# Kernel optimization log

Hardware: AMD Instinct MI355X
Metric: run time of the kernel (lower is better)

Reference implementation:

```python
import jax, jax.numpy as jnp
import numpy as np

EMBED = 512
WINDOW = 64

def setup_inputs() -> dict:
    key = jax.random.key(0)
    ks = jax.random.split(key, 5)
    B, S, E = 4, 4096, EMBED
    s = 1.0 / np.sqrt(E)
    x = jax.random.normal(ks[0], (B, S, E), dtype=jnp.float32)
    W_qkv = jax.random.uniform(ks[1], (E, 3 * E), minval=-s, maxval=s, dtype=jnp.float32)
    b_qkv = jax.random.uniform(ks[2], (3 * E,), minval=-s, maxval=s, dtype=jnp.float32)
    W_out = jax.random.uniform(ks[3], (E, E), minval=-s, maxval=s, dtype=jnp.float32)
    b_out = jax.random.uniform(ks[4], (E,), minval=-s, maxval=s, dtype=jnp.float32)
    return {"x": x, "W_qkv": W_qkv, "b_qkv": b_qkv, "W_out": W_out, "b_out": b_out}

def reference(x, W_qkv, b_qkv, W_out, b_out):
    B, S, E = x.shape
    scale = jnp.sqrt(jnp.asarray(E, dtype=x.dtype))
    qkv = x @ W_qkv + b_qkv                    # [B,S,3E]
    q, k, v = jnp.split(qkv, 3, axis=-1)       # each [B,S,E]
    scores = jnp.einsum('bqe,bke->bqk', q, k) / scale  # [B,S,S]
    pos = jnp.arange(S)
    dist = pos[None, :] - pos[:, None]         # [S,S]
    window_mask = jnp.abs(dist) <= WINDOW
    neg_inf = jnp.asarray(-jnp.inf, dtype=scores.dtype)
    scores = jnp.where(window_mask[None, :, :], scores, neg_inf)
    attn = jax.nn.softmax(scores, axis=-1)     # every row has in-window entries
    attended = jnp.einsum('bqk,bke->bqe', attn, v)
    return attended @ W_out + b_out
```

## Files before the change

### kernel.cpp

```cpp
#include <hip/hip_runtime.h>

typedef __attribute__((ext_vector_type(8))) _Float16 f16x8;
typedef __attribute__((ext_vector_type(4))) _Float16 f16x4;
typedef __attribute__((ext_vector_type(4))) float f32x4;
typedef __attribute__((address_space(1))) const char gc_char;
typedef __attribute__((address_space(3))) char ls_char;

#define MFMA(a, b, c) __builtin_amdgcn_mfma_f32_16x16x32_f16((a), (b), (c), 0, 0, 0)
#define FENCE() asm volatile("" ::: "memory")
#define BARRIER() do { FENCE(); __builtin_amdgcn_s_barrier(); FENCE(); } while (0)
#define VMW(n) asm volatile("s_waitcnt vmcnt(" #n ")" ::: "memory")

static constexpr int SEQ = 4096;
static constexpr int EMB = 512;
static constexpr float QSCALE = 0.04419417382415922f;

__device__ __forceinline__ void gl_lds16(const void* g, void* l) {
    __builtin_amdgcn_global_load_lds((gc_char*)g, (ls_char*)l, 16, 0, 0);
}

__global__ void k_prep(const float* __restrict__ x, _Float16* __restrict__ xb,
                       const float* __restrict__ Wq, _Float16* __restrict__ WqT,
                       const float* __restrict__ Wo, _Float16* __restrict__ WoT) {
    const int bid = blockIdx.x, tid = threadIdx.x;
    if (bid < 4096) {
        long i = (long)bid * 256 + tid;
        const float4* p = (const float4*)x + i * 2;
        float4 a = p[0], b = p[1];
        f16x8 v;
        v[0] = (_Float16)a.x; v[1] = (_Float16)a.y; v[2] = (_Float16)a.z; v[3] = (_Float16)a.w;
        v[4] = (_Float16)b.x; v[5] = (_Float16)b.y; v[6] = (_Float16)b.z; v[7] = (_Float16)b.w;
        *(f16x8*)(xb + i * 8) = v;
    } else {
        __shared__ float Ls[64][65];
        int t = bid - 4096;
        const float* W; _Float16* WT; int N, k0, n0;
        if (t < 192) { W = Wq; WT = WqT; N = 1536; k0 = (t & 7) * 64; n0 = (t >> 3) * 64; }
        else { t -= 192; W = Wo; WT = WoT; N = 512; k0 = (t & 7) * 64; n0 = (t >> 3) * 64; }
        int c = tid & 63, r4 = tid >> 6;
#pragma unroll
        for (int i = 0; i < 16; ++i) {
            int row = i * 4 + r4;
            Ls[row][c] = W[(long)(k0 + row) * N + n0 + c];
        }
        __syncthreads();
#pragma unroll
        for (int i = 0; i < 16; ++i) {
            int row = i * 4 + r4;
            WT[(long)(n0 + row) * 512 + k0 + c] = (_Float16)Ls[c][row];
        }
    }
}

__launch_bounds__(512, 2) __global__
void k_gemm_qkv(const _Float16* __restrict__ A, const _Float16* __restrict__ BT,
                const float* __restrict__ bias,
                _Float16* __restrict__ Qo, _Float16* __restrict__ Ko, _Float16* __restrict__ VT) {
    extern __shared__ __align__(16) char smem[];
    const int tid = threadIdx.x, w = tid >> 6, lane = tid & 63, g = lane >> 4, f = lane & 15;
    const int wrow = w >> 2, wcol = w & 3;
    const int bid = blockIdx.x;
    const int swz = (bid & 7) * 48 + (bid >> 3);
    const int brow = swz / 6, bcol = swz - brow * 6;
    const long row0 = (long)brow * 256;
    const int col0 = bcol * 256;
    const char* Abase = (const char*)A + row0 * 1024;
    const char* Bbase = (const char*)BT + (long)col0 * 1024;

    f32x4 acc[8][4] = {};
    f16x8 a[4][2], b[2][2];

    auto stageA = [&](int h, char* dstbuf, int kt) {
#pragma unroll
        for (int it = 0; it < 2; ++it) {
            int s = it * 512 + tid;
            int lr = s >> 3;
            int ch = (s & 7) ^ (lr & 7);
            int r = (lr & 63) | ((lr & 64) << 1) | (h << 6);
            gl_lds16(Abase + (long)r * 1024 + kt * 128 + ch * 16, dstbuf + h * 16384 + s * 16);
        }
    };
    auto stageB = [&](int h, char* dstbuf, int kt) {
#pragma unroll
        for (int it = 0; it < 2; ++it) {
            int s = it * 512 + tid;
            int lr = s >> 3;
            int ch = (s & 7) ^ (lr & 7);
            int n = (lr & 31) | ((lr >> 5) << 6) | (h << 5);
            gl_lds16(Bbase + (long)n * 1024 + kt * 128 + ch * 16, dstbuf + h * 16384 + s * 16);
        }
    };
    auto ldA = [&](const char* buf, int mq) {
#pragma unroll
        for (int mi = 0; mi < 4; ++mi)
#pragma unroll
            for (int ks = 0; ks < 2; ++ks) {
                int r = wrow * 128 + mq * 64 + mi * 16 + f;
                int half = (r >> 6) & 1, lr = (r & 63) | ((r & 128) >> 1);
                int cl = ks * 4 + g;
                a[mi][ks] = *(const f16x8*)(buf + half * 16384 + lr * 128 + ((cl ^ (lr & 7)) << 4));
            }
    };
    auto ldB = [&](const char* buf, int nq) {
#pragma unroll
        for (int ni = 0; ni < 2; ++ni)
#pragma unroll
            for (int ks = 0; ks < 2; ++ks) {
                int n = wcol * 64 + nq * 32 + ni * 16 + f;
                int half = (n >> 5) & 1, lr = (n & 31) | (((n >> 6) & 3) << 5);
                int cl = ks * 4 + g;
                b[ni][ks] = *(const f16x8*)(buf + half * 16384 + lr * 128 + ((cl ^ (lr & 7)) << 4));
            }
    };
    auto mfma16 = [&](int mq, int nq) {
        __builtin_amdgcn_s_setprio(1);
#pragma unroll
        for (int mi = 0; mi < 4; ++mi)
#pragma unroll
            for (int ni = 0; ni < 2; ++ni)
#pragma unroll
                for (int ks = 0; ks < 2; ++ks)
                    acc[mq * 4 + mi][nq * 2 + ni] = MFMA(a[mi][ks], b[ni][ks], acc[mq * 4 + mi][nq * 2 + ni]);
        __builtin_amdgcn_s_setprio(0);
    };

    {
        char* A0 = smem;
        char* B0 = smem + 32768;
        stageA(0, A0, 0); stageB(0, B0, 0); stageB(1, B0, 0); stageA(1, A0, 0);
    }
    VMW(4);
    BARRIER();

    for (int kt = 0; kt < 8; ++kt) {
        const char* Ac = smem + (kt & 1) * 65536;
        const char* Bc = Ac + 32768;
        char* An = smem + ((kt + 1) & 1) * 65536;
        char* Bn = An + 32768;
        const bool last = (kt == 7);
        ldA(Ac, 0); ldB(Bc, 0);
        if (!last) stageA(0, An, kt + 1);
        BARRIER();
        mfma16(0, 0);
        if (!last) { VMW(4); } else { VMW(2); }
        BARRIER();
        ldB(Bc, 1);
        if (!last) stageB(0, Bn, kt + 1);
        BARRIER();
        mfma16(0, 1);
        if (!last) { VMW(4); } else { VMW(0); }
        BARRIER();
        ldA(Ac, 1); ldB(Bc, 0);
        if (!last) stageB(1, Bn, kt + 1);
        BARRIER();
        mfma16(1, 0);
        BARRIER();
        ldB(Bc, 1);
        if (!last) stageA(1, An, kt + 1);
        BARRIER();
        mfma16(1, 1);
        if (!last) { VMW(4); }
        BARRIER();
    }

    float bv[4];
#pragma unroll
    for (int ni = 0; ni < 4; ++ni) bv[ni] = bias[col0 + wcol * 64 + ni * 16 + f];

    if (col0 >= 1024) {
#pragma unroll
        for (int mi = 0; mi < 8; ++mi)
#pragma unroll
            for (int ni = 0; ni < 4; ++ni) {
                int r0 = wrow * 128 + mi * 16 + g * 4;
                int c = wcol * 64 + ni * 16 + f;
                f16x4 v4;
#pragma unroll
                for (int j = 0; j < 4; ++j) v4[j] = (_Float16)(acc[mi][ni][j] + bv[ni]);
                *(f16x4*)(smem + c * 512 + ((r0 * 2) ^ ((c & 7) << 4))) = v4;
            }
        __syncthreads();
        int bb = (int)(row0 >> 12);
        _Float16* vt = VT + ((long)bb * 512 + (col0 - 1024)) * 4096 + (row0 & 4095);
#pragma unroll
        for (int it = 0; it < 16; ++it) {
            int e = it * 16 + (tid >> 5);
            int ch = tid & 31;
            f16x8 v = *(const f16x8*)(smem + e * 512 + ((ch * 16) ^ ((e & 7) << 4)));
            *(f16x8*)(vt + (long)e * 4096 + ch * 8) = v;
        }
    } else {
        const float sc = (col0 < 512) ? QSCALE : 1.0f;
#pragma unroll
        for (int mi = 0; mi < 8; ++mi)
#pragma unroll
            for (int ni = 0; ni < 4; ++ni)
#pragma unroll
                for (int j = 0; j < 4; ++j) {
                    int r = wrow * 128 + mi * 16 + g * 4 + j;
                    int c = wcol * 64 + ni * 16 + f;
                    float v = (acc[mi][ni][j] + bv[ni]) * sc;
                    int pc = ((c >> 3) + ((r >> 2) & 7) * 2) & 31;
                    *(_Float16*)(smem + r * 512 + pc * 16 + (c & 7) * 2) = (_Float16)v;
                }
        __syncthreads();
        _Float16* dst = (col0 < 512) ? Qo : Ko;
        int cofs = (col0 < 512) ? col0 : col0 - 512;
#pragma unroll
        for (int it = 0; it < 16; ++it) {
            int r = it * 16 + (tid >> 5);
            int ch = tid & 31;
            int pc = (ch + ((r >> 2) & 7) * 2) & 31;
            f16x8 v = *(const f16x8*)(smem + r * 512 + pc * 16);
            *(f16x8*)(dst + (row0 + r) * 512 + cofs + ch * 8) = v;
        }
    }
}

__launch_bounds__(256, 2) __global__
void k_gemm_out(const _Float16* __restrict__ A, const _Float16* __restrict__ BT,
                const float* __restrict__ bias, float* __restrict__ out) {
    __shared__ __align__(16) _Float16 As[128 * 64];
    __shared__ __align__(16) _Float16 Bs[128 * 64];
    const int tid = threadIdx.x, w = tid >> 6, lane = tid & 63, g = lane >> 4, f = lane & 15;
    const int wr = w >> 1, wc = w & 1;
    const long row0 = (long)blockIdx.x * 128, col0 = (long)blockIdx.y * 128;
    f32x4 acc[4][4] = {};
    const char* Ab = (const char*)(A + row0 * 512);
    const char* Bb = (const char*)(BT + col0 * 512);

    for (int kt = 0; kt < 8; ++kt) {
        __syncthreads();
        const char* Asrc = Ab + kt * 128;
        const char* Bsrc = Bb + kt * 128;
#pragma unroll
        for (int it = 0; it < 4; ++it) {
            int slot = it * 256 + tid;
            int r = slot >> 3, ch = slot & 7;
            int scol = (ch * 16) ^ ((r & 7) << 4);
            gl_lds16(Asrc + (long)r * 1024 + scol, (char*)As + (it * 256 + (tid & 0xC0)) * 16);
            gl_lds16(Bsrc + (long)r * 1024 + scol, (char*)Bs + (it * 256 + (tid & 0xC0)) * 16);
        }
        __syncthreads();
#pragma unroll
        for (int ks = 0; ks < 2; ++ks) {
            f16x8 af[4], bf[4];
#pragma unroll
            for (int mi = 0; mi < 4; ++mi) {
                int r = wr * 64 + mi * 16 + f;
                af[mi] = *(const f16x8*)((const char*)As + r * 128 + ((ks * 64 + g * 16) ^ ((r & 7) << 4)));
            }
#pragma unroll
            for (int ni = 0; ni < 4; ++ni) {
                int r = wc * 64 + ni * 16 + f;
                bf[ni] = *(const f16x8*)((const char*)Bs + r * 128 + ((ks * 64 + g * 16) ^ ((r & 7) << 4)));
            }
#pragma unroll
            for (int mi = 0; mi < 4; ++mi)
#pragma unroll
                for (int ni = 0; ni < 4; ++ni)
                    acc[mi][ni] = MFMA(af[mi], bf[ni], acc[mi][ni]);
        }
    }
#pragma unroll
    for (int mi = 0; mi < 4; ++mi)
#pragma unroll
        for (int ni = 0; ni < 4; ++ni) {
            long r0 = row0 + wr * 64 + mi * 16 + g * 4;
            int c = (int)col0 + wc * 64 + ni * 16 + f;
            float bv = bias[c];
#pragma unroll
            for (int j = 0; j < 4; ++j)
                out[(r0 + j) * 512 + c] = acc[mi][ni][j] + bv;
        }
}

__launch_bounds__(512, 1) __global__
void k_attn(const _Float16* __restrict__ Qb, const _Float16* __restrict__ Kb,
            const _Float16* __restrict__ VT, _Float16* __restrict__ Ob) {
    extern __shared__ __align__(16) char smem[];
    char* buf[2] = { smem, smem + 49152 };
    char* Pl = smem + 98304;
    float* Mp = (float*)(smem + 123904);
    float* Lp = (float*)(smem + 124928);

    const int tid = threadIdx.x, w = tid >> 6, lane = tid & 63, g = lane >> 4, f = lane & 15;
    const int rh = w >> 2, kh = w & 3;
    const int bid = blockIdx.x;
    const int swzb = (bid & 7) * 32 + (bid >> 3);
    const int b = swzb >> 6, qt = swzb & 63;
    const int q0 = qt * 64, kbase = q0 - 64;
    const long bofs = (long)b * SEQ;

    f16x8 qf[2][16];
#pragma unroll
    for (int mt = 0; mt < 2; ++mt) {
        const _Float16* qr = Qb + (bofs + q0 + rh * 32 + mt * 16 + f) * EMB + g * 8;
#pragma unroll
        for (int ks = 0; ks < 16; ++ks) qf[mt][ks] = *(const f16x8*)(qr + ks * 32);
    }

    auto stageK = [&](int ec, char* dst) {
#pragma unroll
        for (int it = 0; it < 6; ++it) {
            int slot = it * 512 + tid;
            int r = slot >> 4, c = slot & 15;
            int cs = c ^ (r & 7);
            int key = min(max(kbase + r, 0), SEQ - 1);
            gl_lds16(Kb + (bofs + key) * EMB + ec * 128 + cs * 8, dst + slot * 16);
        }
    };
    auto stageVT = [&](int ec, char* dst) {
#pragma unroll
        for (int it = 0; it < 6; ++it) {
            int slot = it * 512 + tid;
            int r = slot / 24, c = slot - r * 24;
            int cs = c ^ (r & 7);
            int k0 = min(max(kbase + cs * 8, 0), SEQ - 8);
            gl_lds16(VT + ((long)b * 512 + ec * 128 + r) * 4096 + k0, dst + slot * 16);
        }
    };

    f32x4 sacc[2][3] = {};
    stageK(0, buf[0]);
    __syncthreads();
    for (int ec = 0; ec < 4; ++ec) {
        if (ec < 3) stageK(ec + 1, buf[(ec + 1) & 1]);
        else stageVT(0, buf[0]);
        const char* kb = buf[ec & 1];
#pragma unroll
        for (int kk = 0; kk < 4; ++kk) {
#pragma unroll
            for (int t = 0; t < 3; ++t) {
                int n = kh * 48 + t * 16 + f;
                f16x8 bf = *(const f16x8*)(kb + n * 256 + (((kk * 4 + g) ^ (n & 7)) << 4));
#pragma unroll
                for (int mt = 0; mt < 2; ++mt)
                    sacc[mt][t] = MFMA(qf[mt][ec * 4 + kk], bf, sacc[mt][t]);
            }
        }
        __syncthreads();
    }

    float m[2][4] = {{-3e30f, -3e30f, -3e30f, -3e30f}, {-3e30f, -3e30f, -3e30f, -3e30f}};
    float l[2][4] = {};
#pragma unroll
    for (int mt = 0; mt < 2; ++mt)
#pragma unroll
        for (int t = 0; t < 3; ++t) {
            int key = kbase + kh * 48 + t * 16 + f;
            bool kv = (key >= 0) && (key < SEQ);
#pragma unroll
            for (int j = 0; j < 4; ++j) {
                int d = key - (q0 + rh * 32 + mt * 16 + g * 4 + j);
                bool valid = kv && (d >= -64) && (d <= 64);
                float s = valid ? sacc[mt][t][j] : -3e30f;
                sacc[mt][t][j] = s;
                m[mt][j] = fmaxf(m[mt][j], s);
            }
        }
#pragma unroll
    for (int mt = 0; mt < 2; ++mt)
#pragma unroll
        for (int j = 0; j < 4; ++j) {
            m[mt][j] = fmaxf(m[mt][j], __shfl_xor(m[mt][j], 1));
            m[mt][j] = fmaxf(m[mt][j], __shfl_xor(m[mt][j], 2));
            m[mt][j] = fmaxf(m[mt][j], __shfl_xor(m[mt][j], 4));
            m[mt][j] = fmaxf(m[mt][j], __shfl_xor(m[mt][j], 8));
        }
    if (f == 0) {
#pragma unroll
        for (int mt = 0; mt < 2; ++mt)
#pragma unroll
            for (int j = 0; j < 4; ++j)
                Mp[kh * 64 + rh * 32 + mt * 16 + g * 4 + j] = m[mt][j];
    }
    __syncthreads();
#pragma unroll
    for (int mt = 0; mt < 2; ++mt)
#pragma unroll
        for (int j = 0; j < 4; ++j) {
            int r = rh * 32 + mt * 16 + g * 4 + j;
            m[mt][j] = fmaxf(fmaxf(Mp[r], Mp[64 + r]), fmaxf(Mp[128 + r], Mp[192 + r]));
        }
#pragma unroll
    for (int mt = 0; mt < 2; ++mt)
#pragma unroll
        for (int t = 0; t < 3; ++t)
#pragma unroll
            for (int j = 0; j < 4; ++j) {
                float p = __expf(sacc[mt][t][j] - m[mt][j]);
                sacc[mt][t][j] = p;
                l[mt][j] += p;
            }
#pragma unroll
    for (int mt = 0; mt < 2; ++mt)
#pragma unroll
        for (int j = 0; j < 4; ++j) {
            l[mt][j] += __shfl_xor(l[mt][j], 1);
            l[mt][j] += __shfl_xor(l[mt][j], 2);
            l[mt][j] += __shfl_xor(l[mt][j], 4);
            l[mt][j] += __shfl_xor(l[mt][j], 8);
        }
    if (f == 0) {
#pragma unroll
        for (int mt = 0; mt < 2; ++mt)
#pragma unroll
            for (int j = 0; j < 4; ++j)
                Lp[kh * 64 + rh * 32 + mt * 16 + g * 4 + j] = l[mt][j];
    }
#pragma unroll
    for (int mt = 0; mt < 2; ++mt)
#pragma unroll
        for (int t = 0; t < 3; ++t)
#pragma unroll
            for (int j = 0; j < 4; ++j)
                *(_Float16*)(Pl + (rh * 32 + mt * 16 + g * 4 + j) * 400 +
                             (kh * 48 + t * 16 + f) * 2) = (_Float16)sacc[mt][t][j];
    __syncthreads();

    float rl[2][4];
#pragma unroll
    for (int mt = 0; mt < 2; ++mt)
#pragma unroll
        for (int j = 0; j < 4; ++j) {
            int r = rh * 32 + mt * 16 + g * 4 + j;
            rl[mt][j] = 1.0f / (Lp[r] + Lp[64 + r] + Lp[128 + r] + Lp[192 + r]);
        }

    f16x8 pf[2][6];
#pragma unroll
    for (int mt = 0; mt < 2; ++mt)
#pragma unroll
        for (int kc = 0; kc < 6; ++kc)
            pf[mt][kc] = *(const f16x8*)(Pl + (rh * 32 + mt * 16 + f) * 400 + kc * 64 + g * 16);

    for (int ec = 0; ec < 4; ++ec) {
        if (ec < 3) stageVT(ec + 1, buf[(ec + 1) & 1]);
        const char* vb = buf[ec & 1];
        f32x4 o[2][2] = {};
#pragma unroll
        for (int kc = 0; kc < 6; ++kc) {
#pragma unroll
            for (int nt = 0; nt < 2; ++nt) {
                int e = kh * 32 + nt * 16 + f;
                f16x8 vf = *(const f16x8*)(vb + e * 384 + (((kc * 4 + g) ^ (e & 7)) << 4));
#pragma unroll
                for (int mt = 0; mt < 2; ++mt)
                    o[mt][nt] = MFMA(pf[mt][kc], vf, o[mt][nt]);
            }
        }
#pragma unroll
        for (int mt = 0; mt < 2; ++mt)
#pragma unroll
            for (int nt = 0; nt < 2; ++nt) {
                _Float16* ob = Ob + (bofs + q0 + rh * 32 + mt * 16 + g * 4) * EMB +
                               ec * 128 + kh * 32 + nt * 16 + f;
#pragma unroll
                for (int j = 0; j < 4; ++j)
                    ob[(long)j * EMB] = (_Float16)(o[mt][nt][j] * rl[mt][j]);
            }
        if (ec < 3) __syncthreads();
    }
}

extern "C" void kernel_launch(void* const* d_in, const int* in_sizes, int n_in,
                              void* d_out, int out_size, void* d_ws, size_t ws_size,
                              hipStream_t stream) {
    const float* x     = (const float*)d_in[0];
    const float* W_qkv = (const float*)d_in[1];
    const float* b_qkv = (const float*)d_in[2];
    const float* W_out = (const float*)d_in[3];
    const float* b_out = (const float*)d_in[4];

    char* ws = (char*)d_ws;
    _Float16* xb    = (_Float16*)(ws);
    _Float16* WqkvT = (_Float16*)(ws + 16777216);
    _Float16* WoutT = (_Float16*)(ws + 16777216 + 1572864);
    _Float16* Qb    = (_Float16*)(ws + 18874368);
    _Float16* Kb    = (_Float16*)(ws + 18874368 + 16777216);
    _Float16* VT    = (_Float16*)(ws + 18874368 + 33554432);
    _Float16* Ob    = xb;
    float* out = (float*)d_out;

    (void)hipFuncSetAttribute((const void*)k_gemm_qkv,
                              hipFuncAttributeMaxDynamicSharedMemorySize, 131072);
    (void)hipFuncSetAttribute((const void*)k_attn,
                              hipFuncAttributeMaxDynamicSharedMemorySize, 126976);

    k_prep<<<4352, 256, 0, stream>>>(x, xb, W_qkv, WqkvT, W_out, WoutT);
    k_gemm_qkv<<<384, 512, 131072, stream>>>(xb, WqkvT, b_qkv, Qb, Kb, VT);
    k_attn<<<256, 512, 125952, stream>>>(Qb, Kb, VT, Ob);
    dim3 g2(128, 4);
    k_gemm_out<<<g2, 256, 0, stream>>>(Ob, WoutT, b_out, out);
}
```

Measured before the change: 87.61 us.

## Unify GEMMs into templated 128x256-tile pipelined kernel for QKV and output projections

Replaces the QKV GEMM (256x256 tiles, 384 blocks) and the simple output GEMM with one templated kernel that uses 128x256 tiles and a double-buffered global_load_lds pipeline. The QKV projection now launches 768 blocks to fill more CUs, and the output projection gains the async staged pipeline in place of its synchronous per-k-step loads. In exchange each tile reuses its operands less and issues more loads per FLOP, and occupancy is set to one block per CU.

```diff
diff --git a/kernel.cpp b/kernel.cpp
--- a/kernel.cpp
+++ b/kernel.cpp
@@ -52,227 +52,175 @@
     }
 }
 
-__launch_bounds__(512, 2) __global__
-void k_gemm_qkv(const _Float16* __restrict__ A, const _Float16* __restrict__ BT,
-                const float* __restrict__ bias,
-                _Float16* __restrict__ Qo, _Float16* __restrict__ Ko, _Float16* __restrict__ VT) {
+template <int NCT, int EPI>
+__launch_bounds__(512, 1) __global__
+void k_gemm2(const _Float16* __restrict__ A, const _Float16* __restrict__ BT,
+             const float* __restrict__ bias, void* o0, void* o1, void* o2) {
     extern __shared__ __align__(16) char smem[];
-    const int tid = threadIdx.x, w = tid >> 6, lane = tid & 63, g = lane >> 4, f = lane & 15;
+    const int tid = threadIdx.x, lane = tid & 63, w = tid >> 6, g = lane >> 4, f = lane & 15;
     const int wrow = w >> 2, wcol = w & 3;
     const int bid = blockIdx.x;
-    const int swz = (bid & 7) * 48 + (bid >> 3);
-    const int brow = swz / 6, bcol = swz - brow * 6;
-    const long row0 = (long)brow * 256;
+    constexpr int NBLK = 128 * NCT;
+    const int swz = (bid & 7) * (NBLK / 8) + (bid >> 3);
+    const int brow = swz / NCT, bcol = swz - brow * NCT;
+    const long row0 = (long)brow * 128;
     const int col0 = bcol * 256;
     const char* Abase = (const char*)A + row0 * 1024;
     const char* Bbase = (const char*)BT + (long)col0 * 1024;
 
-    f32x4 acc[8][4] = {};
-    f16x8 a[4][2], b[2][2];
-
-    auto stageA = [&](int h, char* dstbuf, int kt) {
+    f32x4 acc[4][4] = {};
+    f16x8 a[2][2], breg[2][2][2];
+
+    auto stageA = [&](int h, char* dst, int kt) {
+        int rr = tid >> 3;
+        int ch = (tid & 7) ^ (rr & 7);
+        int grow = h * 32 + (rr & 31) + (rr >> 5) * 64;
+        gl_lds16(Abase + (long)grow * 1024 + kt * 128 + ch * 16, dst + h * 8192 + tid * 16);
+    };
+    auto stageB = [&](int h, char* dst, int kt) {
 #pragma unroll
         for (int it = 0; it < 2; ++it) {
             int s = it * 512 + tid;
-            int lr = s >> 3;
-            int ch = (s & 7) ^ (lr & 7);
-            int r = (lr & 63) | ((lr & 64) << 1) | (h << 6);
-            gl_lds16(Abase + (long)r * 1024 + kt * 128 + ch * 16, dstbuf + h * 16384 + s * 16);
-        }
-    };
-    auto stageB = [&](int h, char* dstbuf, int kt) {
-#pragma unroll
-        for (int it = 0; it < 2; ++it) {
-            int s = it * 512 + tid;
-            int lr = s >> 3;
-            int ch = (s & 7) ^ (lr & 7);
-            int n = (lr & 31) | ((lr >> 5) << 6) | (h << 5);
-            gl_lds16(Bbase + (long)n * 1024 + kt * 128 + ch * 16, dstbuf + h * 16384 + s * 16);
-        }
-    };
-    auto ldA = [&](const char* buf, int mq) {
+            int cc = s >> 3;
+            int ch = (s & 7) ^ (cc & 7);
+            int gcol = h * 32 + (cc & 31) + (cc >> 5) * 64;
+            gl_lds16(Bbase + (long)gcol * 1024 + kt * 128 + ch * 16,
+                     dst + 16384 + h * 16384 + s * 16);
+        }
+    };
+    auto ldA = [&](const char* buf, int mh) {
+#pragma unroll
+        for (int mi = 0; mi < 2; ++mi)
+#pragma unroll
+            for (int ks = 0; ks < 2; ++ks) {
+                int rr = wrow * 32 + mi * 16 + f;
+                int cl = ks * 4 + g;
+                a[mi][ks] = *(const f16x8*)(buf + mh * 8192 + rr * 128 + ((cl ^ (rr & 7)) << 4));
+            }
+    };
+    auto ldB = [&](const char* buf, int nh) {
+#pragma unroll
+        for (int ni = 0; ni < 2; ++ni)
+#pragma unroll
+            for (int ks = 0; ks < 2; ++ks) {
+                int cc = wcol * 32 + ni * 16 + f;
+                int cl = ks * 4 + g;
+                breg[nh][ni][ks] =
+                    *(const f16x8*)(buf + 16384 + nh * 16384 + cc * 128 + ((cl ^ (cc & 7)) << 4));
+            }
+    };
+    auto mfma8 = [&](int mh, int nh) {
+        __builtin_amdgcn_s_setprio(1);
+#pragma unroll
+        for (int mi = 0; mi < 2; ++mi)
+#pragma unroll
+            for (int ni = 0; ni < 2; ++ni)
+#pragma unroll
+                for (int ks = 0; ks < 2; ++ks)
+                    acc[mh * 2 + mi][nh * 2 + ni] =
+                        MFMA(a[mi][ks], breg[nh][ni][ks], acc[mh * 2 + mi][nh * 2 + ni]);
+        __builtin_amdgcn_s_setprio(0);
+    };
+
+    stageB(0, smem, 0);
+    stageA(0, smem, 0); stageA(1, smem, 0);
+    stageB(1, smem, 0);
+    VMW(3);
+    BARRIER();
+
+    for (int kt = 0; kt < 8; ++kt) {
+        const char* cur = smem + (kt & 1) * 49152;
+        char* nxt = smem + ((kt + 1) & 1) * 49152;
+        const bool last = (kt == 7);
+        ldA(cur, 0); ldB(cur, 0);
+        if (!last) stageB(0, nxt, kt + 1);
+        BARRIER();
+        mfma8(0, 0);
+        if (!last) { VMW(2); } else { VMW(0); }
+        BARRIER();
+        ldB(cur, 1);
+        if (!last) { stageA(0, nxt, kt + 1); stageA(1, nxt, kt + 1); }
+        BARRIER();
+        mfma8(0, 1);
+        BARRIER();
+        ldA(cur, 1);
+        if (!last) stageB(1, nxt, kt + 1);
+        BARRIER();
+        mfma8(1, 0);
+        BARRIER();
+        mfma8(1, 1);
+        if (!last) { VMW(3); }
+        BARRIER();
+    }
+
+    if (EPI == 1) {
+        float* out = (float*)o0;
 #pragma unroll
         for (int mi = 0; mi < 4; ++mi)
 #pragma unroll
-            for (int ks = 0; ks < 2; ++ks) {
-                int r = wrow * 128 + mq * 64 + mi * 16 + f;
-                int half = (r >> 6) & 1, lr = (r & 63) | ((r & 128) >> 1);
-                int cl = ks * 4 + g;
-                a[mi][ks] = *(const f16x8*)(buf + half * 16384 + lr * 128 + ((cl ^ (lr & 7)) << 4));
-            }
-    };
-    auto ldB = [&](const char* buf, int nq) {
-#pragma unroll
-        for (int ni = 0; ni < 2; ++ni)
-#pragma unroll
-            for (int ks = 0; ks < 2; ++ks) {
-                int n = wcol * 64 + nq * 32 + ni * 16 + f;
-                int half = (n >> 5) & 1, lr = (n & 31) | (((n >> 6) & 3) << 5);
-                int cl = ks * 4 + g;
-                b[ni][ks] = *(const f16x8*)(buf + half * 16384 + lr * 128 + ((cl ^ (lr & 7)) << 4));
-            }
-    };
-    auto mfma16 = [&](int mq, int nq) {
-        __builtin_amdgcn_s_setprio(1);
+            for (int ni = 0; ni < 4; ++ni) {
+                long r0 = row0 + wrow * 64 + mi * 16 + g * 4;
+                int c = col0 + wcol * 64 + ni * 16 + f;
+                float bv = bias[c];
+#pragma unroll
+                for (int j = 0; j < 4; ++j)
+                    out[(r0 + j) * 512 + c] = acc[mi][ni][j] + bv;
+            }
+        return;
+    }
+
+    float bv[4];
+#pragma unroll
+    for (int ni = 0; ni < 4; ++ni) bv[ni] = bias[col0 + wcol * 64 + ni * 16 + f];
+
+    if (col0 >= 1024) {
 #pragma unroll
         for (int mi = 0; mi < 4; ++mi)
 #pragma unroll
-            for (int ni = 0; ni < 2; ++ni)
-#pragma unroll
-                for (int ks = 0; ks < 2; ++ks)
-                    acc[mq * 4 + mi][nq * 2 + ni] = MFMA(a[mi][ks], b[ni][ks], acc[mq * 4 + mi][nq * 2 + ni]);
-        __builtin_amdgcn_s_setprio(0);
-    };
-
-    {
-        char* A0 = smem;
-        char* B0 = smem + 32768;
-        stageA(0, A0, 0); stageB(0, B0, 0); stageB(1, B0, 0); stageA(1, A0, 0);
-    }
-    VMW(4);
-    BARRIER();
-
-    for (int kt = 0; kt < 8; ++kt) {
-        const char* Ac = smem + (kt & 1) * 65536;
-        const char* Bc = Ac + 32768;
-        char* An = smem + ((kt + 1) & 1) * 65536;
-        char* Bn = An + 32768;
-        const bool last = (kt == 7);
-        ldA(Ac, 0); ldB(Bc, 0);
-        if (!last) stageA(0, An, kt + 1);
-        BARRIER();
-        mfma16(0, 0);
-        if (!last) { VMW(4); } else { VMW(2); }
-        BARRIER();
-        ldB(Bc, 1);
-        if (!last) stageB(0, Bn, kt + 1);
-        BARRIER();
-        mfma16(0, 1);
-        if (!last) { VMW(4); } else { VMW(0); }
-        BARRIER();
-        ldA(Ac, 1); ldB(Bc, 0);
-        if (!last) stageB(1, Bn, kt + 1);
-        BARRIER();
-        mfma16(1, 0);
-        BARRIER();
-        ldB(Bc, 1);
-        if (!last) stageA(1, An, kt + 1);
-        BARRIER();
-        mfma16(1, 1);
-        if (!last) { VMW(4); }
-        BARRIER();
-    }
-
-    float bv[4];
-#pragma unroll
-    for (int ni = 0; ni < 4; ++ni) bv[ni] = bias[col0 + wcol * 64 + ni * 16 + f];
-
-    if (col0 >= 1024) {
-#pragma unroll
-        for (int mi = 0; mi < 8; ++mi)
-#pragma unroll
             for (int ni = 0; ni < 4; ++ni) {
-                int r0 = wrow * 128 + mi * 16 + g * 4;
+                int r0 = wrow * 64 + mi * 16 + g * 4;
                 int c = wcol * 64 + ni * 16 + f;
                 f16x4 v4;
 #pragma unroll
                 for (int j = 0; j < 4; ++j) v4[j] = (_Float16)(acc[mi][ni][j] + bv[ni]);
-                *(f16x4*)(smem + c * 512 + ((r0 * 2) ^ ((c & 7) << 4))) = v4;
+                *(f16x4*)(smem + c * 256 + ((r0 * 2) ^ ((c & 7) << 4))) = v4;
             }
         __syncthreads();
         int bb = (int)(row0 >> 12);
-        _Float16* vt = VT + ((long)bb * 512 + (col0 - 1024)) * 4096 + (row0 & 4095);
-#pragma unroll
-        for (int it = 0; it < 16; ++it) {
-            int e = it * 16 + (tid >> 5);
-            int ch = tid & 31;
-            f16x8 v = *(const f16x8*)(smem + e * 512 + ((ch * 16) ^ ((e & 7) << 4)));
+        _Float16* vt = (_Float16*)o2 + ((long)bb * 512 + (col0 - 1024)) * 4096 + (row0 & 4095);
+#pragma unroll
+        for (int it = 0; it < 8; ++it) {
+            int slot = it * 512 + tid;
+            int e = slot >> 4, ch = slot & 15;
+            f16x8 v = *(const f16x8*)(smem + e * 256 + ((ch * 16) ^ ((e & 7) << 4)));
             *(f16x8*)(vt + (long)e * 4096 + ch * 8) = v;
         }
     } else {
         const float sc = (col0 < 512) ? QSCALE : 1.0f;
 #pragma unroll
-        for (int mi = 0; mi < 8; ++mi)
+        for (int mi = 0; mi < 4; ++mi)
 #pragma unroll
             for (int ni = 0; ni < 4; ++ni)
 #pragma unroll
                 for (int j = 0; j < 4; ++j) {
-                    int r = wrow * 128 + mi * 16 + g * 4 + j;
+                    int r = wrow * 64 + mi * 16 + g * 4 + j;
                     int c = wcol * 64 + ni * 16 + f;
                     float v = (acc[mi][ni][j] + bv[ni]) * sc;
                     int pc = ((c >> 3) + ((r >> 2) & 7) * 2) & 31;
                     *(_Float16*)(smem + r * 512 + pc * 16 + (c & 7) * 2) = (_Float16)v;
                 }
         __syncthreads();
-        _Float16* dst = (col0 < 512) ? Qo : Ko;
+        _Float16* dst = (col0 < 512) ? (_Float16*)o0 : (_Float16*)o1;
         int cofs = (col0 < 512) ? col0 : col0 - 512;
 #pragma unroll
-        for (int it = 0; it < 16; ++it) {
-            int r = it * 16 + (tid >> 5);
-            int ch = tid & 31;
+        for (int it = 0; it < 8; ++it) {
+            int slot = it * 512 + tid;
+            int r = slot >> 5, ch = slot & 31;
             int pc = (ch + ((r >> 2) & 7) * 2) & 31;
             f16x8 v = *(const f16x8*)(smem + r * 512 + pc * 16);
             *(f16x8*)(dst + (row0 + r) * 512 + cofs + ch * 8) = v;
         }
     }
-}
-
-__launch_bounds__(256, 2) __global__
-void k_gemm_out(const _Float16* __restrict__ A, const _Float16* __restrict__ BT,
-                const float* __restrict__ bias, float* __restrict__ out) {
-    __shared__ __align__(16) _Float16 As[128 * 64];
-    __shared__ __align__(16) _Float16 Bs[128 * 64];
-    const int tid = threadIdx.x, w = tid >> 6, lane = tid & 63, g = lane >> 4, f = lane & 15;
-    const int wr = w >> 1, wc = w & 1;
-    const long row0 = (long)blockIdx.x * 128, col0 = (long)blockIdx.y * 128;
-    f32x4 acc[4][4] = {};
-    const char* Ab = (const char*)(A + row0 * 512);
-    const char* Bb = (const char*)(BT + col0 * 512);
-
-    for (int kt = 0; kt < 8; ++kt) {
-        __syncthreads();
-        const char* Asrc = Ab + kt * 128;
-        const char* Bsrc = Bb + kt * 128;
-#pragma unroll
-        for (int it = 0; it < 4; ++it) {
-            int slot = it * 256 + tid;
-            int r = slot >> 3, ch = slot & 7;
-            int scol = (ch * 16) ^ ((r & 7) << 4);
-            gl_lds16(Asrc + (long)r * 1024 + scol, (char*)As + (it * 256 + (tid & 0xC0)) * 16);
-            gl_lds16(Bsrc + (long)r * 1024 + scol, (char*)Bs + (it * 256 + (tid & 0xC0)) * 16);
-        }
-        __syncthreads();
-#pragma unroll
-        for (int ks = 0; ks < 2; ++ks) {
-            f16x8 af[4], bf[4];
-#pragma unroll
-            for (int mi = 0; mi < 4; ++mi) {
-                int r = wr * 64 + mi * 16 + f;
-                af[mi] = *(const f16x8*)((const char*)As + r * 128 + ((ks * 64 + g * 16) ^ ((r & 7) << 4)));
-            }
-#pragma unroll
-            for (int ni = 0; ni < 4; ++ni) {
-                int r = wc * 64 + ni * 16 + f;
-                bf[ni] = *(const f16x8*)((const char*)Bs + r * 128 + ((ks * 64 + g * 16) ^ ((r & 7) << 4)));
-            }
-#pragma unroll
-            for (int mi = 0; mi < 4; ++mi)
-#pragma unroll
-                for (int ni = 0; ni < 4; ++ni)
-                    acc[mi][ni] = MFMA(af[mi], bf[ni], acc[mi][ni]);
-        }
-    }
-#pragma unroll
-    for (int mi = 0; mi < 4; ++mi)
-#pragma unroll
-        for (int ni = 0; ni < 4; ++ni) {
-            long r0 = row0 + wr * 64 + mi * 16 + g * 4;
-            int c = (int)col0 + wc * 64 + ni * 16 + f;
-            float bv = bias[c];
-#pragma unroll
-            for (int j = 0; j < 4; ++j)
-                out[(r0 + j) * 512 + c] = acc[mi][ni][j] + bv;
-        }
 }
 
 __launch_bounds__(512, 1) __global__
@@ -483,14 +431,15 @@
     _Float16* Ob    = xb;
     float* out = (float*)d_out;
 
-    (void)hipFuncSetAttribute((const void*)k_gemm_qkv,
-                              hipFuncAttributeMaxDynamicSharedMemorySize, 131072);
+    (void)hipFuncSetAttribute((const void*)k_gemm2<6, 0>,
+                              hipFuncAttributeMaxDynamicSharedMemorySize, 98304);
+    (void)hipFuncSetAttribute((const void*)k_gemm2<2, 1>,
+                              hipFuncAttributeMaxDynamicSharedMemorySize, 98304);
     (void)hipFuncSetAttribute((const void*)k_attn,
                               hipFuncAttributeMaxDynamicSharedMemorySize, 126976);
 
     k_prep<<<4352, 256, 0, stream>>>(x, xb, W_qkv, WqkvT, W_out, WoutT);
-    k_gemm_qkv<<<384, 512, 131072, stream>>>(xb, WqkvT, b_qkv, Qb, Kb, VT);
+    k_gemm2<6, 0><<<768, 512, 98304, stream>>>(xb, WqkvT, b_qkv, Qb, Kb, VT);
     k_attn<<<256, 512, 125952, stream>>>(Qb, Kb, VT, Ob);
-    dim3 g2(128, 4);
-    k_gemm_out<<<g2, 256, 0, stream>>>(Ob, WoutT, b_out, out);
+    k_gemm2<2, 1><<<256, 512, 98304, stream>>>(Ob, WoutT, b_out, out, nullptr, nullptr);
 }
```

Result: faster. 82.43 us (-5.9%).
